# Optimization experiments

Hardware: AMD Instinct MI355X
Metric: run time of the kernel (lower is better)

Reference implementation:

```python
import jax, jax.numpy as jnp
import numpy as np


def _hilbert_d2xy(n, d):
    # standard Hilbert curve: distance d -> (x, y) on n x n grid (n power of 2)
    x = y = 0
    t = d
    s = 1
    while s < n:
        rx = 1 & (t // 2)
        ry = 1 & (t ^ rx)
        if ry == 0:
            if rx == 1:
                x = s - 1 - x
                y = s - 1 - y
            x, y = y, x
        x += s * rx
        y += s * ry
        t //= 4
        s *= 2
    return x, y


def _hilbert_perm(seq_len):
    n = int(round(np.sqrt(seq_len)))
    assert n * n == seq_len
    perm = np.empty(seq_len, dtype=np.int32)
    for d in range(seq_len):
        x, y = _hilbert_d2xy(n, d)
        perm[d] = y * n + x  # linear (row-major) index visited at Hilbert step d
    return perm


def setup_inputs() -> dict:
    key = jax.random.key(0)
    k1, k2, k3 = jax.random.split(key, 3)
    B, S, H, D = 1, 4096, 8, 64
    q = jax.random.normal(k1, (B, S, H, D), dtype=jnp.float32)
    k = jax.random.normal(k2, (B, S, H, D), dtype=jnp.float32)
    v = jax.random.normal(k3, (B, S, H, D), dtype=jnp.float32)
    hilbert_perm = jnp.asarray(_hilbert_perm(S))
    return {"q": q, "k": k, "v": v, "hilbert_perm": hilbert_perm}


def reference(q, k, v, hilbert_perm):
    B, S, H, D = q.shape
    inv_perm = jnp.argsort(hilbert_perm)

    # apply_hilbert_ordering along dim=1 (seq): gather by permutation
    q_o = q[:, hilbert_perm]
    k_o = k[:, hilbert_perm]
    v_o = v[:, hilbert_perm]

    # faithful to original: raw flat reshape of [B,S,H,D] -> [B*H, S, D]
    q_f = q_o.reshape(B * H, S, D)
    k_f = k_o.reshape(B * H, S, D)
    v_f = v_o.reshape(B * H, S, D)

    scale = 1.0 / jnp.sqrt(jnp.asarray(D, dtype=q.dtype))
    scores = jnp.einsum('bsd,btd->bst', q_f, k_f) * scale  # [B*H, S, S]
    attn = jax.nn.softmax(scores, axis=-1)
    out_f = jnp.einsum('bst,btd->bsd', attn, v_f)  # [B*H, S, D]

    out = out_f.reshape(B, H, S, D).transpose(0, 2, 1, 3).reshape(B, S, H, D)
    # inverse Hilbert ordering along dim=1
    return out[:, inv_perm]
```

## Files before the change

### kernel.cpp

```cpp
#include <hip/hip_runtime.h>

typedef _Float16 f16;
typedef _Float16 f16x4 __attribute__((ext_vector_type(4)));
typedef _Float16 f16x8 __attribute__((ext_vector_type(8)));
typedef __fp16 fp16x2 __attribute__((ext_vector_type(2)));
typedef float f32x4 __attribute__((ext_vector_type(4)));

#define MFMA_16x16x32_F16(A, B, C) __builtin_amdgcn_mfma_f32_16x16x32_f16((A), (B), (C), 0, 0, 0)

typedef const __attribute__((address_space(1))) char gchar;
typedef __attribute__((address_space(3))) char lchar;

__device__ __forceinline__ float fexp2(float x) { return __builtin_amdgcn_exp2f(x); }
__device__ __forceinline__ int swzb(int b) { return b ^ ((b >> 3) & 0x70); }

namespace {
constexpr int SB = 4096;
constexpr size_t BB = (size_t)SB * 64 * 2;
}

__global__ __launch_bounds__(256)
void hilbert_prepass_kernel(const float* __restrict__ kp, const float* __restrict__ vp,
                            const int* __restrict__ perm,
                            char* __restrict__ kw, char* __restrict__ vtw)
{
    const int bid = blockIdx.x;
    const int batch = bid & 7;
    const int tile = bid >> 3;
    const int tid = (int)threadIdx.x;
    const int r = tid >> 2;
    const int c4 = tid & 3;

    __shared__ float Vl[64][68];

    const int t = tile * 64 + r;
    const int srow = perm[batch * 512 + (t >> 3)];
    const size_t boff = (size_t)srow * 512 + (t & 7) * 64 + c4 * 16;

    {
        const float* ks = kp + boff;
        const float4 k0 = *(const float4*)(ks + 0);
        const float4 k1 = *(const float4*)(ks + 4);
        const float4 k2 = *(const float4*)(ks + 8);
        const float4 k3 = *(const float4*)(ks + 12);
        f16x8 h0, h1;
        h0[0] = (f16)k0.x; h0[1] = (f16)k0.y; h0[2] = (f16)k0.z; h0[3] = (f16)k0.w;
        h0[4] = (f16)k1.x; h0[5] = (f16)k1.y; h0[6] = (f16)k1.z; h0[7] = (f16)k1.w;
        h1[0] = (f16)k2.x; h1[1] = (f16)k2.y; h1[2] = (f16)k2.z; h1[3] = (f16)k2.w;
        h1[4] = (f16)k3.x; h1[5] = (f16)k3.y; h1[6] = (f16)k3.z; h1[7] = (f16)k3.w;
        char* kt = kw + (size_t)batch * BB + (size_t)tile * 8192;
        const int o = r * 128 + c4 * 32;
        *(f16x8*)(kt + swzb(o)) = h0;
        *(f16x8*)(kt + swzb(o + 16)) = h1;
    }
    {
        const float* vs = vp + boff;
        *(float4*)&Vl[r][c4 * 16 + 0]  = *(const float4*)(vs + 0);
        *(float4*)&Vl[r][c4 * 16 + 4]  = *(const float4*)(vs + 4);
        *(float4*)&Vl[r][c4 * 16 + 8]  = *(const float4*)(vs + 8);
        *(float4*)&Vl[r][c4 * 16 + 12] = *(const float4*)(vs + 12);
    }
    __syncthreads();
    {
        const int d = tid >> 2;
        const int tq = (tid & 3) * 16;
        f16x8 a, b;
#pragma unroll
        for (int j = 0; j < 8; ++j) a[j] = (f16)Vl[tq + j][d];
#pragma unroll
        for (int j = 0; j < 8; ++j) b[j] = (f16)Vl[tq + 8 + j][d];
        char* vt = vtw + (size_t)batch * BB + (size_t)tile * 8192;
        const int o = d * 128 + tq * 2;
        *(f16x8*)(vt + swzb(o)) = a;
        *(f16x8*)(vt + swzb(o + 16)) = b;
    }
}

__global__ __launch_bounds__(512, 4)
void hilbert_attn_kernel(const float* __restrict__ qp,
                         const int* __restrict__ perm,
                         const char* __restrict__ kw, const char* __restrict__ vtw,
                         float* __restrict__ op)
{
    __shared__ __align__(16) char SM[81920];

    const int bid = blockIdx.x;
    const int batch = bid & 7;
    const int qbase = (bid >> 3) * 64;
    const int tid = (int)threadIdx.x;
    const int w = tid >> 6;
    const int lane = tid & 63;
    const int l16 = lane & 15;
    const int g = lane >> 4;
    const int half = w >> 2;
    const int wq = w & 3;
    const int swz = (l16 & 7) << 4;

    f16x8 Qf[2];
    {
        const int t = qbase + wq * 16 + l16;
        const int srow = perm[batch * 512 + (t >> 3)];
        const float* src = qp + (size_t)srow * 512 + (t & 7) * 64 + g * 8;
        constexpr float qscl = 0.125f * 1.44269504088896340736f;
#pragma unroll
        for (int kt = 0; kt < 2; ++kt) {
            const float4 x0 = *(const float4*)(src + 32 * kt);
            const float4 x1 = *(const float4*)(src + 32 * kt + 4);
            f16x8 f;
            f[0] = (f16)(x0.x * qscl); f[1] = (f16)(x0.y * qscl);
            f[2] = (f16)(x0.z * qscl); f[3] = (f16)(x0.w * qscl);
            f[4] = (f16)(x1.x * qscl); f[5] = (f16)(x1.y * qscl);
            f[6] = (f16)(x1.z * qscl); f[7] = (f16)(x1.w * qscl);
            Qf[kt] = f;
        }
    }

    f32x4 oacc[4];
#pragma unroll
    for (int i = 0; i < 4; ++i) oacc[i] = (f32x4){0.f, 0.f, 0.f, 0.f};
    float lrun = 0.f;

    const char* ksrc = kw + (size_t)batch * BB + (size_t)tid * 16;
    const char* vsrc = vtw + (size_t)batch * BB + (size_t)tid * 16;
    char* pbase = &SM[65536 + w * 2048];

    {
        lchar* dst = (lchar*)&SM[w << 10];
        __builtin_amdgcn_global_load_lds((gchar*)(ksrc), dst, 16, 0, 0);
        __builtin_amdgcn_global_load_lds((gchar*)(ksrc + 8192), dst + 8192, 16, 0, 0);
        __builtin_amdgcn_global_load_lds((gchar*)(vsrc), dst + 16384, 16, 0, 0);
        __builtin_amdgcn_global_load_lds((gchar*)(vsrc + 8192), dst + 24576, 16, 0, 0);
    }
    __syncthreads();

    for (int it = 0; it < 32; ++it) {
        const int cur = it & 1;
        const int kbb = cur * 32768 + half * 8192;
        const int vbb = cur * 32768 + 16384 + half * 8192;

        if (it < 31) {
            const size_t go = (size_t)(it + 1) * 16384;
            lchar* dst = (lchar*)&SM[(cur ^ 1) * 32768 + (w << 10)];
            __builtin_amdgcn_global_load_lds((gchar*)(ksrc + go), dst, 16, 0, 0);
            __builtin_amdgcn_global_load_lds((gchar*)(ksrc + go + 8192), dst + 8192, 16, 0, 0);
            __builtin_amdgcn_global_load_lds((gchar*)(vsrc + go), dst + 16384, 16, 0, 0);
            __builtin_amdgcn_global_load_lds((gchar*)(vsrc + go + 8192), dst + 24576, 16, 0, 0);
        }

        f32x4 sa[4];
#pragma unroll
        for (int i = 0; i < 4; ++i) sa[i] = (f32x4){0.f, 0.f, 0.f, 0.f};
#pragma unroll
        for (int kt = 0; kt < 2; ++kt) {
#pragma unroll
            for (int mt = 0; mt < 4; ++mt) {
                const int off = kbb + (l16 + 16 * mt) * 128 + (((g + 4 * kt) * 16) ^ swz);
                const f16x8 kf = *(const f16x8*)&SM[off];
                sa[mt] = MFMA_16x16x32_F16(kf, Qf[kt], sa[mt]);
            }
        }

#pragma unroll
        for (int mt = 0; mt < 4; ++mt) {
            const float p0 = fexp2(sa[mt][0]);
            const float p1 = fexp2(sa[mt][1]);
            const float p2 = fexp2(sa[mt][2]);
            const float p3 = fexp2(sa[mt][3]);
            lrun += (p0 + p1) + (p2 + p3);
            union { f16x4 v; fp16x2 h[2]; } u;
            u.h[0] = __builtin_amdgcn_cvt_pkrtz(p0, p1);
            u.h[1] = __builtin_amdgcn_cvt_pkrtz(p2, p3);
            const int poff = l16 * 128 + (((2 * mt + (g >> 1)) ^ (l16 & 7)) << 4) + (g & 1) * 8;
            *(f16x4*)&pbase[poff] = u.v;
        }

#pragma unroll
        for (int kt = 0; kt < 2; ++kt) {
            const int poff = l16 * 128 + (((g + 4 * kt) ^ (l16 & 7)) << 4);
            const f16x8 pf = *(const f16x8*)&pbase[poff];
#pragma unroll
            for (int mtd = 0; mtd < 4; ++mtd) {
                const int voff = vbb + (l16 + 16 * mtd) * 128 + (((g + 4 * kt) * 16) ^ swz);
                const f16x8 vf = *(const f16x8*)&SM[voff];
                oacc[mtd] = MFMA_16x16x32_F16(vf, pf, oacc[mtd]);
            }
        }

        __syncthreads();
    }

    lrun += __shfl_xor(lrun, 16);
    lrun += __shfl_xor(lrun, 32);

    float* OB = (float*)SM;
    float* ML = (float*)&SM[16384];
    if (w >= 4) {
        float* ob = OB + (w - 4) * 1024;
#pragma unroll
        for (int mtd = 0; mtd < 4; ++mtd)
            *(f32x4*)&ob[l16 * 64 + mtd * 16 + g * 4] = oacc[mtd];
        if (g == 0) ML[(w - 4) * 16 + l16] = lrun;
    }
    __syncthreads();
    if (w < 4) {
        const float linv = 1.f / (lrun + ML[w * 16 + l16]);
        float* ob = OB + w * 1024;

        const int t = qbase + wq * 16 + l16;
        const int srow = perm[t];
        float* dst = op + (size_t)srow * 512 + batch * 64 + 4 * g;
#pragma unroll
        for (int mtd = 0; mtd < 4; ++mtd) {
            const f32x4 o2 = *(const f32x4*)&ob[l16 * 64 + mtd * 16 + g * 4];
            float4 o;
            o.x = (oacc[mtd][0] + o2[0]) * linv;
            o.y = (oacc[mtd][1] + o2[1]) * linv;
            o.z = (oacc[mtd][2] + o2[2]) * linv;
            o.w = (oacc[mtd][3] + o2[3]) * linv;
            *(float4*)(dst + 16 * mtd) = o;
        }
    }
}

extern "C" void kernel_launch(void* const* d_in, const int* in_sizes, int n_in,
                              void* d_out, int out_size, void* d_ws, size_t ws_size,
                              hipStream_t stream) {
    (void)in_sizes; (void)n_in; (void)out_size; (void)ws_size;
    const float* q = (const float*)d_in[0];
    const float* k = (const float*)d_in[1];
    const float* v = (const float*)d_in[2];
    const int* perm = (const int*)d_in[3];
    float* out = (float*)d_out;
    char* kw = (char*)d_ws;
    char* vtw = kw + 8 * BB;
    hipLaunchKernelGGL(hilbert_prepass_kernel, dim3(512), dim3(256), 0, stream,
                       k, v, perm, kw, vtw);
    hipLaunchKernelGGL(hilbert_attn_kernel, dim3(512), dim3(512), 0, stream,
                       q, perm, kw, vtw, out);
}
```

Measured before the change: 60.84 us.

## Process two query sub-tiles per wave to reuse K/V LDS fragments

Each workgroup now handles 128 query rows instead of 64, with every wave computing two 16-row query sub-tiles that share the same K and V fragments read from LDS. The grid halves to 256 blocks, so K/V global-to-LDS traffic per query row and LDS reads per MFMA are halved. The cost is more registers per thread (two sets of accumulators and Q fragments), a larger LDS footprint, a lower occupancy bound, and fewer blocks than a large GPU may have compute units, which can leave some idle.

```diff
diff --git a/kernel.cpp b/kernel.cpp
--- a/kernel.cpp
+++ b/kernel.cpp
@@ -76,17 +76,17 @@
     }
 }
 
-__global__ __launch_bounds__(512, 4)
+__global__ __launch_bounds__(512, 2)
 void hilbert_attn_kernel(const float* __restrict__ qp,
                          const int* __restrict__ perm,
                          const char* __restrict__ kw, const char* __restrict__ vtw,
                          float* __restrict__ op)
 {
-    __shared__ __align__(16) char SM[81920];
+    __shared__ __align__(16) char SM[98304];
 
     const int bid = blockIdx.x;
     const int batch = bid & 7;
-    const int qbase = (bid >> 3) * 64;
+    const int qbase = (bid >> 3) * 128;
     const int tid = (int)threadIdx.x;
     const int w = tid >> 6;
     const int lane = tid & 63;
@@ -96,33 +96,39 @@
     const int wq = w & 3;
     const int swz = (l16 & 7) << 4;
 
-    f16x8 Qf[2];
-    {
-        const int t = qbase + wq * 16 + l16;
-        const int srow = perm[batch * 512 + (t >> 3)];
-        const float* src = qp + (size_t)srow * 512 + (t & 7) * 64 + g * 8;
+    f16x8 Qf0[2], Qf1[2];
+    {
         constexpr float qscl = 0.125f * 1.44269504088896340736f;
 #pragma unroll
-        for (int kt = 0; kt < 2; ++kt) {
-            const float4 x0 = *(const float4*)(src + 32 * kt);
-            const float4 x1 = *(const float4*)(src + 32 * kt + 4);
-            f16x8 f;
-            f[0] = (f16)(x0.x * qscl); f[1] = (f16)(x0.y * qscl);
-            f[2] = (f16)(x0.z * qscl); f[3] = (f16)(x0.w * qscl);
-            f[4] = (f16)(x1.x * qscl); f[5] = (f16)(x1.y * qscl);
-            f[6] = (f16)(x1.z * qscl); f[7] = (f16)(x1.w * qscl);
-            Qf[kt] = f;
-        }
-    }
-
-    f32x4 oacc[4];
-#pragma unroll
-    for (int i = 0; i < 4; ++i) oacc[i] = (f32x4){0.f, 0.f, 0.f, 0.f};
-    float lrun = 0.f;
+        for (int s = 0; s < 2; ++s) {
+            const int t = qbase + wq * 32 + s * 16 + l16;
+            const int srow = perm[batch * 512 + (t >> 3)];
+            const float* src = qp + (size_t)srow * 512 + (t & 7) * 64 + g * 8;
+#pragma unroll
+            for (int kt = 0; kt < 2; ++kt) {
+                const float4 x0 = *(const float4*)(src + 32 * kt);
+                const float4 x1 = *(const float4*)(src + 32 * kt + 4);
+                f16x8 f;
+                f[0] = (f16)(x0.x * qscl); f[1] = (f16)(x0.y * qscl);
+                f[2] = (f16)(x0.z * qscl); f[3] = (f16)(x0.w * qscl);
+                f[4] = (f16)(x1.x * qscl); f[5] = (f16)(x1.y * qscl);
+                f[6] = (f16)(x1.z * qscl); f[7] = (f16)(x1.w * qscl);
+                if (s == 0) Qf0[kt] = f; else Qf1[kt] = f;
+            }
+        }
+    }
+
+    f32x4 oacc0[4], oacc1[4];
+#pragma unroll
+    for (int i = 0; i < 4; ++i) {
+        oacc0[i] = (f32x4){0.f, 0.f, 0.f, 0.f};
+        oacc1[i] = (f32x4){0.f, 0.f, 0.f, 0.f};
+    }
+    float lr0 = 0.f, lr1 = 0.f;
 
     const char* ksrc = kw + (size_t)batch * BB + (size_t)tid * 16;
     const char* vsrc = vtw + (size_t)batch * BB + (size_t)tid * 16;
-    char* pbase = &SM[65536 + w * 2048];
+    char* pbase = &SM[65536 + w * 4096];
 
     {
         lchar* dst = (lchar*)&SM[w << 10];
@@ -147,77 +153,104 @@
             __builtin_amdgcn_global_load_lds((gchar*)(vsrc + go + 8192), dst + 24576, 16, 0, 0);
         }
 
-        f32x4 sa[4];
-#pragma unroll
-        for (int i = 0; i < 4; ++i) sa[i] = (f32x4){0.f, 0.f, 0.f, 0.f};
+        f32x4 sa0[4], sa1[4];
+#pragma unroll
+        for (int i = 0; i < 4; ++i) {
+            sa0[i] = (f32x4){0.f, 0.f, 0.f, 0.f};
+            sa1[i] = (f32x4){0.f, 0.f, 0.f, 0.f};
+        }
 #pragma unroll
         for (int kt = 0; kt < 2; ++kt) {
 #pragma unroll
             for (int mt = 0; mt < 4; ++mt) {
                 const int off = kbb + (l16 + 16 * mt) * 128 + (((g + 4 * kt) * 16) ^ swz);
                 const f16x8 kf = *(const f16x8*)&SM[off];
-                sa[mt] = MFMA_16x16x32_F16(kf, Qf[kt], sa[mt]);
+                sa0[mt] = MFMA_16x16x32_F16(kf, Qf0[kt], sa0[mt]);
+                sa1[mt] = MFMA_16x16x32_F16(kf, Qf1[kt], sa1[mt]);
             }
         }
 
 #pragma unroll
         for (int mt = 0; mt < 4; ++mt) {
-            const float p0 = fexp2(sa[mt][0]);
-            const float p1 = fexp2(sa[mt][1]);
-            const float p2 = fexp2(sa[mt][2]);
-            const float p3 = fexp2(sa[mt][3]);
-            lrun += (p0 + p1) + (p2 + p3);
+            const float a0 = fexp2(sa0[mt][0]);
+            const float a1 = fexp2(sa0[mt][1]);
+            const float a2 = fexp2(sa0[mt][2]);
+            const float a3 = fexp2(sa0[mt][3]);
+            lr0 += (a0 + a1) + (a2 + a3);
             union { f16x4 v; fp16x2 h[2]; } u;
-            u.h[0] = __builtin_amdgcn_cvt_pkrtz(p0, p1);
-            u.h[1] = __builtin_amdgcn_cvt_pkrtz(p2, p3);
+            u.h[0] = __builtin_amdgcn_cvt_pkrtz(a0, a1);
+            u.h[1] = __builtin_amdgcn_cvt_pkrtz(a2, a3);
             const int poff = l16 * 128 + (((2 * mt + (g >> 1)) ^ (l16 & 7)) << 4) + (g & 1) * 8;
             *(f16x4*)&pbase[poff] = u.v;
+
+            const float b0 = fexp2(sa1[mt][0]);
+            const float b1 = fexp2(sa1[mt][1]);
+            const float b2 = fexp2(sa1[mt][2]);
+            const float b3 = fexp2(sa1[mt][3]);
+            lr1 += (b0 + b1) + (b2 + b3);
+            union { f16x4 v; fp16x2 h[2]; } u2;
+            u2.h[0] = __builtin_amdgcn_cvt_pkrtz(b0, b1);
+            u2.h[1] = __builtin_amdgcn_cvt_pkrtz(b2, b3);
+            *(f16x4*)&pbase[2048 + poff] = u2.v;
         }
 
 #pragma unroll
         for (int kt = 0; kt < 2; ++kt) {
             const int poff = l16 * 128 + (((g + 4 * kt) ^ (l16 & 7)) << 4);
-            const f16x8 pf = *(const f16x8*)&pbase[poff];
+            const f16x8 pf0 = *(const f16x8*)&pbase[poff];
+            const f16x8 pf1 = *(const f16x8*)&pbase[2048 + poff];
 #pragma unroll
             for (int mtd = 0; mtd < 4; ++mtd) {
                 const int voff = vbb + (l16 + 16 * mtd) * 128 + (((g + 4 * kt) * 16) ^ swz);
                 const f16x8 vf = *(const f16x8*)&SM[voff];
-                oacc[mtd] = MFMA_16x16x32_F16(vf, pf, oacc[mtd]);
+                oacc0[mtd] = MFMA_16x16x32_F16(vf, pf0, oacc0[mtd]);
+                oacc1[mtd] = MFMA_16x16x32_F16(vf, pf1, oacc1[mtd]);
             }
         }
 
         __syncthreads();
     }
 
-    lrun += __shfl_xor(lrun, 16);
-    lrun += __shfl_xor(lrun, 32);
+    lr0 += __shfl_xor(lr0, 16);
+    lr0 += __shfl_xor(lr0, 32);
+    lr1 += __shfl_xor(lr1, 16);
+    lr1 += __shfl_xor(lr1, 32);
 
     float* OB = (float*)SM;
-    float* ML = (float*)&SM[16384];
+    float* ML = (float*)&SM[32768];
     if (w >= 4) {
-        float* ob = OB + (w - 4) * 1024;
-#pragma unroll
-        for (int mtd = 0; mtd < 4; ++mtd)
-            *(f32x4*)&ob[l16 * 64 + mtd * 16 + g * 4] = oacc[mtd];
-        if (g == 0) ML[(w - 4) * 16 + l16] = lrun;
+        float* ob = OB + wq * 2048;
+#pragma unroll
+        for (int mtd = 0; mtd < 4; ++mtd) {
+            *(f32x4*)&ob[l16 * 64 + mtd * 16 + g * 4] = oacc0[mtd];
+            *(f32x4*)&ob[(16 + l16) * 64 + mtd * 16 + g * 4] = oacc1[mtd];
+        }
+        if (g == 0) {
+            ML[wq * 32 + l16] = lr0;
+            ML[wq * 32 + 16 + l16] = lr1;
+        }
     }
     __syncthreads();
     if (w < 4) {
-        const float linv = 1.f / (lrun + ML[w * 16 + l16]);
-        float* ob = OB + w * 1024;
-
-        const int t = qbase + wq * 16 + l16;
-        const int srow = perm[t];
-        float* dst = op + (size_t)srow * 512 + batch * 64 + 4 * g;
-#pragma unroll
-        for (int mtd = 0; mtd < 4; ++mtd) {
-            const f32x4 o2 = *(const f32x4*)&ob[l16 * 64 + mtd * 16 + g * 4];
-            float4 o;
-            o.x = (oacc[mtd][0] + o2[0]) * linv;
-            o.y = (oacc[mtd][1] + o2[1]) * linv;
-            o.z = (oacc[mtd][2] + o2[2]) * linv;
-            o.w = (oacc[mtd][3] + o2[3]) * linv;
-            *(float4*)(dst + 16 * mtd) = o;
+        float* ob = OB + wq * 2048;
+#pragma unroll
+        for (int s = 0; s < 2; ++s) {
+            const float lmine = (s == 0) ? lr0 : lr1;
+            const float linv = 1.f / (lmine + ML[wq * 32 + s * 16 + l16]);
+            const int t = qbase + wq * 32 + s * 16 + l16;
+            const int srow = perm[t];
+            float* dst = op + (size_t)srow * 512 + batch * 64 + 4 * g;
+#pragma unroll
+            for (int mtd = 0; mtd < 4; ++mtd) {
+                const f32x4 mine = (s == 0) ? oacc0[mtd] : oacc1[mtd];
+                const f32x4 o2 = *(const f32x4*)&ob[(s * 16 + l16) * 64 + mtd * 16 + g * 4];
+                float4 o;
+                o.x = (mine[0] + o2[0]) * linv;
+                o.y = (mine[1] + o2[1]) * linv;
+                o.z = (mine[2] + o2[2]) * linv;
+                o.w = (mine[3] + o2[3]) * linv;
+                *(float4*)(dst + 16 * mtd) = o;
+            }
         }
     }
 }
@@ -235,6 +268,6 @@
     char* vtw = kw + 8 * BB;
     hipLaunchKernelGGL(hilbert_prepass_kernel, dim3(512), dim3(256), 0, stream,
                        k, v, perm, kw, vtw);
-    hipLaunchKernelGGL(hilbert_attn_kernel, dim3(512), dim3(512), 0, stream,
+    hipLaunchKernelGGL(hilbert_attn_kernel, dim3(256), dim3(512), 0, stream,
                        q, perm, kw, vtw, out);
 }
```

Result: faster. 56.74 us (-6.7%).

## Switch attention to 32x32x16 MFMA with register-resident P and split K/V staging

Applied to the files above, without the earlier changes.

Replaces the 16x16x32 MFMA tiling with 32x32x16 MFMAs, doubling the query rows per block to 128 and halving the grid. The V prepass layout is permuted so the exp'd scores can feed the PV MFMA straight from registers, removing the per-wave LDS round trip for P. K and V global-to-LDS staging are now issued separately with explicit vmcnt waits, raw barriers and setprio around the MFMA phases, and the last iteration is peeled. Larger tiles raise register pressure (launch bounds drop to 2 blocks) and leave fewer blocks than CUs.

```diff
diff --git a/kernel.cpp b/kernel.cpp
--- a/kernel.cpp
+++ b/kernel.cpp
@@ -5,8 +5,9 @@
 typedef _Float16 f16x8 __attribute__((ext_vector_type(8)));
 typedef __fp16 fp16x2 __attribute__((ext_vector_type(2)));
 typedef float f32x4 __attribute__((ext_vector_type(4)));
-
-#define MFMA_16x16x32_F16(A, B, C) __builtin_amdgcn_mfma_f32_16x16x32_f16((A), (B), (C), 0, 0, 0)
+typedef float f32x16 __attribute__((ext_vector_type(16)));
+
+#define MFMA32(A, B, C) __builtin_amdgcn_mfma_f32_32x32x16_f16((A), (B), (C), 0, 0, 0)
 
 typedef const __attribute__((address_space(1))) char gchar;
 typedef __attribute__((address_space(3))) char lchar;
@@ -18,6 +19,7 @@
 constexpr int SB = 4096;
 constexpr size_t BB = (size_t)SB * 64 * 2;
 }
+
 
 __global__ __launch_bounds__(256)
 void hilbert_prepass_kernel(const float* __restrict__ kp, const float* __restrict__ vp,
@@ -63,66 +65,126 @@
     __syncthreads();
     {
         const int d = tid >> 2;
-        const int tq = (tid & 3) * 16;
-        f16x8 a, b;
-#pragma unroll
-        for (int j = 0; j < 8; ++j) a[j] = (f16)Vl[tq + j][d];
-#pragma unroll
-        for (int j = 0; j < 8; ++j) b[j] = (f16)Vl[tq + 8 + j][d];
+        const int a = tid & 3;
         char* vt = vtw + (size_t)batch * BB + (size_t)tile * 8192;
-        const int o = d * 128 + tq * 2;
-        *(f16x8*)(vt + swzb(o)) = a;
-        *(f16x8*)(vt + swzb(o + 16)) = b;
+        const int sbase = 32 * (a >> 1) + 16 * (a & 1);
+#pragma unroll
+        for (int gp = 0; gp < 4; ++gp) {
+            f16x4 qv;
+#pragma unroll
+            for (int v = 0; v < 4; ++v) qv[v] = (f16)Vl[16 * a + 4 * gp + v][d];
+            const int slot = sbase + 8 * (gp & 1) + 4 * (gp >> 1);
+            *(f16x4*)(vt + swzb(d * 128 + slot * 2)) = qv;
+        }
     }
 }
 
-__global__ __launch_bounds__(512, 4)
+__global__ __launch_bounds__(512, 2)
 void hilbert_attn_kernel(const float* __restrict__ qp,
                          const int* __restrict__ perm,
                          const char* __restrict__ kw, const char* __restrict__ vtw,
                          float* __restrict__ op)
 {
-    __shared__ __align__(16) char SM[81920];
+    __shared__ __align__(16) char SM[65536];
 
     const int bid = blockIdx.x;
     const int batch = bid & 7;
-    const int qbase = (bid >> 3) * 64;
+    const int qbase = (bid >> 3) * 128;
     const int tid = (int)threadIdx.x;
     const int w = tid >> 6;
     const int lane = tid & 63;
-    const int l16 = lane & 15;
-    const int g = lane >> 4;
+    const int l5 = lane & 31;
+    const int hi = lane >> 5;
+    const int swz = (lane & 7) << 4;
     const int half = w >> 2;
     const int wq = w & 3;
-    const int swz = (l16 & 7) << 4;
-
-    f16x8 Qf[2];
-    {
-        const int t = qbase + wq * 16 + l16;
+
+    const f32x16 Z16 = {0.f, 0.f, 0.f, 0.f, 0.f, 0.f, 0.f, 0.f,
+                        0.f, 0.f, 0.f, 0.f, 0.f, 0.f, 0.f, 0.f};
+
+    f16x8 Qf[4];
+    {
+        constexpr float qscl = 0.125f * 1.44269504088896340736f;
+        const int t = qbase + wq * 32 + l5;
         const int srow = perm[batch * 512 + (t >> 3)];
-        const float* src = qp + (size_t)srow * 512 + (t & 7) * 64 + g * 8;
-        constexpr float qscl = 0.125f * 1.44269504088896340736f;
-#pragma unroll
-        for (int kt = 0; kt < 2; ++kt) {
-            const float4 x0 = *(const float4*)(src + 32 * kt);
-            const float4 x1 = *(const float4*)(src + 32 * kt + 4);
+        const float* src = qp + (size_t)srow * 512 + (t & 7) * 64 + 8 * hi;
+#pragma unroll
+        for (int step = 0; step < 4; ++step) {
+            const float4 x0 = *(const float4*)(src + 16 * step);
+            const float4 x1 = *(const float4*)(src + 16 * step + 4);
             f16x8 f;
             f[0] = (f16)(x0.x * qscl); f[1] = (f16)(x0.y * qscl);
             f[2] = (f16)(x0.z * qscl); f[3] = (f16)(x0.w * qscl);
             f[4] = (f16)(x1.x * qscl); f[5] = (f16)(x1.y * qscl);
             f[6] = (f16)(x1.z * qscl); f[7] = (f16)(x1.w * qscl);
-            Qf[kt] = f;
+            Qf[step] = f;
         }
     }
 
-    f32x4 oacc[4];
-#pragma unroll
-    for (int i = 0; i < 4; ++i) oacc[i] = (f32x4){0.f, 0.f, 0.f, 0.f};
-    float lrun = 0.f;
+    f32x16 oacc[2];
+    oacc[0] = Z16; oacc[1] = Z16;
+    float lr = 0.f;
 
     const char* ksrc = kw + (size_t)batch * BB + (size_t)tid * 16;
     const char* vsrc = vtw + (size_t)batch * BB + (size_t)tid * 16;
-    char* pbase = &SM[65536 + w * 2048];
+
+    union U8 { f16x8 v; fp16x2 h[4]; };
+
+#define STAGE_K(dstbuf, p)                                                           \
+    do {                                                                             \
+        lchar* d_ = (lchar*)&SM[(dstbuf) * 32768 + (w << 10)];                       \
+        const char* s_ = ksrc + (size_t)(p) * 16384;                                 \
+        __builtin_amdgcn_global_load_lds((gchar*)(s_), d_, 16, 0, 0);                \
+        __builtin_amdgcn_global_load_lds((gchar*)(s_ + 8192), d_ + 8192, 16, 0, 0);  \
+    } while (0)
+#define STAGE_V(dstbuf, p)                                                           \
+    do {                                                                             \
+        lchar* d_ = (lchar*)&SM[(dstbuf) * 32768 + 16384 + (w << 10)];               \
+        const char* s_ = vsrc + (size_t)(p) * 16384;                                 \
+        __builtin_amdgcn_global_load_lds((gchar*)(s_), d_, 16, 0, 0);                \
+        __builtin_amdgcn_global_load_lds((gchar*)(s_ + 8192), d_ + 8192, 16, 0, 0);  \
+    } while (0)
+
+#define QK_GRANULE(dst, kbb_, h2)                                                    \
+    do {                                                                             \
+        dst = Z16;                                                                   \
+        _Pragma("unroll")                                                            \
+        for (int step = 0; step < 4; ++step) {                                       \
+            const int off = (kbb_) + (32 * (h2) + l5) * 128 +                        \
+                            ((32 * step + 16 * hi) ^ swz);                           \
+            const f16x8 kf = *(const f16x8*)&SM[off];                                \
+            dst = MFMA32(kf, Qf[step], dst);                                         \
+        }                                                                            \
+    } while (0)
+
+#define SOFTMAX_GRANULE(sa, p0, p1)                                                  \
+    do {                                                                             \
+        float e_[16];                                                                \
+        _Pragma("unroll")                                                            \
+        for (int j = 0; j < 16; ++j) e_[j] = fexp2((sa)[j]);                         \
+        _Pragma("unroll")                                                            \
+        for (int j = 0; j < 16; ++j) lr += e_[j];                                    \
+        _Pragma("unroll")                                                            \
+        for (int i = 0; i < 4; ++i) {                                                \
+            (p0).h[i] = __builtin_amdgcn_cvt_pkrtz(e_[2 * i], e_[2 * i + 1]);        \
+            (p1).h[i] = __builtin_amdgcn_cvt_pkrtz(e_[8 + 2 * i], e_[9 + 2 * i]);    \
+        }                                                                            \
+    } while (0)
+
+#define PV_GRANULE(vbb_, h2, p0, p1)                                                 \
+    do {                                                                             \
+        _Pragma("unroll")                                                            \
+        for (int s = 0; s < 2; ++s) {                                                \
+            const f16x8 pf = s ? (p1).v : (p0).v;                                    \
+            _Pragma("unroll")                                                        \
+            for (int mf = 0; mf < 2; ++mf) {                                         \
+                const int voff = (vbb_) + (32 * mf + l5) * 128 +                     \
+                                 ((64 * (h2) + 32 * s + 16 * hi) ^ swz);             \
+                const f16x8 vf = *(const f16x8*)&SM[voff];                           \
+                oacc[mf] = MFMA32(vf, pf, oacc[mf]);                                 \
+            }                                                                        \
+        }                                                                            \
+    } while (0)
 
     {
         lchar* dst = (lchar*)&SM[w << 10];
@@ -131,94 +193,98 @@
         __builtin_amdgcn_global_load_lds((gchar*)(vsrc), dst + 16384, 16, 0, 0);
         __builtin_amdgcn_global_load_lds((gchar*)(vsrc + 8192), dst + 24576, 16, 0, 0);
     }
-    __syncthreads();
-
-    for (int it = 0; it < 32; ++it) {
+    asm volatile("s_waitcnt vmcnt(0)" ::: "memory");
+    __builtin_amdgcn_s_barrier();
+
+    for (int it = 0; it < 31; ++it) {
         const int cur = it & 1;
         const int kbb = cur * 32768 + half * 8192;
         const int vbb = cur * 32768 + 16384 + half * 8192;
 
-        if (it < 31) {
-            const size_t go = (size_t)(it + 1) * 16384;
-            lchar* dst = (lchar*)&SM[(cur ^ 1) * 32768 + (w << 10)];
-            __builtin_amdgcn_global_load_lds((gchar*)(ksrc + go), dst, 16, 0, 0);
-            __builtin_amdgcn_global_load_lds((gchar*)(ksrc + go + 8192), dst + 8192, 16, 0, 0);
-            __builtin_amdgcn_global_load_lds((gchar*)(vsrc + go), dst + 16384, 16, 0, 0);
-            __builtin_amdgcn_global_load_lds((gchar*)(vsrc + go + 8192), dst + 24576, 16, 0, 0);
-        }
-
-        f32x4 sa[4];
-#pragma unroll
-        for (int i = 0; i < 4; ++i) sa[i] = (f32x4){0.f, 0.f, 0.f, 0.f};
-#pragma unroll
-        for (int kt = 0; kt < 2; ++kt) {
-#pragma unroll
-            for (int mt = 0; mt < 4; ++mt) {
-                const int off = kbb + (l16 + 16 * mt) * 128 + (((g + 4 * kt) * 16) ^ swz);
-                const f16x8 kf = *(const f16x8*)&SM[off];
-                sa[mt] = MFMA_16x16x32_F16(kf, Qf[kt], sa[mt]);
+        STAGE_K(cur ^ 1, it + 1);
+
+        f32x16 sa0, sa1;
+        __builtin_amdgcn_s_setprio(1);
+        QK_GRANULE(sa0, kbb, 0);
+        QK_GRANULE(sa1, kbb, 1);
+        __builtin_amdgcn_s_setprio(0);
+
+        STAGE_V(cur ^ 1, it + 1);
+
+        U8 pa0, pa1, pb0, pb1;
+        SOFTMAX_GRANULE(sa0, pa0, pa1);
+        SOFTMAX_GRANULE(sa1, pb0, pb1);
+
+        asm volatile("s_waitcnt vmcnt(4)" ::: "memory");
+        __builtin_amdgcn_s_barrier();
+
+        __builtin_amdgcn_s_setprio(1);
+        PV_GRANULE(vbb, 0, pa0, pa1);
+        PV_GRANULE(vbb, 1, pb0, pb1);
+        __builtin_amdgcn_s_setprio(0);
+
+        asm volatile("s_waitcnt vmcnt(2)" ::: "memory");
+        __builtin_amdgcn_s_barrier();
+    }
+
+    {
+        const int kbb = 32768 + half * 8192;
+        const int vbb = 32768 + 16384 + half * 8192;
+        f32x16 sa0, sa1;
+        QK_GRANULE(sa0, kbb, 0);
+        QK_GRANULE(sa1, kbb, 1);
+        U8 pa0, pa1, pb0, pb1;
+        SOFTMAX_GRANULE(sa0, pa0, pa1);
+        SOFTMAX_GRANULE(sa1, pb0, pb1);
+        asm volatile("s_waitcnt vmcnt(0)" ::: "memory");
+        __builtin_amdgcn_s_barrier();
+        PV_GRANULE(vbb, 0, pa0, pa1);
+        PV_GRANULE(vbb, 1, pb0, pb1);
+    }
+#undef STAGE_K
+#undef STAGE_V
+#undef QK_GRANULE
+#undef SOFTMAX_GRANULE
+#undef PV_GRANULE
+
+    lr += __shfl_xor(lr, 32);
+
+    __syncthreads();
+
+    float* OB = (float*)SM;
+    float* ML = (float*)&SM[32768];
+    if (w >= 4) {
+        float* ob = OB + wq * 2048;
+#pragma unroll
+        for (int mf = 0; mf < 2; ++mf)
+#pragma unroll
+            for (int q2 = 0; q2 < 4; ++q2) {
+                f32x4 v;
+                v[0] = oacc[mf][4 * q2 + 0]; v[1] = oacc[mf][4 * q2 + 1];
+                v[2] = oacc[mf][4 * q2 + 2]; v[3] = oacc[mf][4 * q2 + 3];
+                *(f32x4*)&ob[l5 * 64 + 32 * mf + 8 * q2 + 4 * hi] = v;
             }
-        }
-
-#pragma unroll
-        for (int mt = 0; mt < 4; ++mt) {
-            const float p0 = fexp2(sa[mt][0]);
-            const float p1 = fexp2(sa[mt][1]);
-            const float p2 = fexp2(sa[mt][2]);
-            const float p3 = fexp2(sa[mt][3]);
-            lrun += (p0 + p1) + (p2 + p3);
-            union { f16x4 v; fp16x2 h[2]; } u;
-            u.h[0] = __builtin_amdgcn_cvt_pkrtz(p0, p1);
-            u.h[1] = __builtin_amdgcn_cvt_pkrtz(p2, p3);
-            const int poff = l16 * 128 + (((2 * mt + (g >> 1)) ^ (l16 & 7)) << 4) + (g & 1) * 8;
-            *(f16x4*)&pbase[poff] = u.v;
-        }
-
-#pragma unroll
-        for (int kt = 0; kt < 2; ++kt) {
-            const int poff = l16 * 128 + (((g + 4 * kt) ^ (l16 & 7)) << 4);
-            const f16x8 pf = *(const f16x8*)&pbase[poff];
-#pragma unroll
-            for (int mtd = 0; mtd < 4; ++mtd) {
-                const int voff = vbb + (l16 + 16 * mtd) * 128 + (((g + 4 * kt) * 16) ^ swz);
-                const f16x8 vf = *(const f16x8*)&SM[voff];
-                oacc[mtd] = MFMA_16x16x32_F16(vf, pf, oacc[mtd]);
-            }
-        }
-
-        __syncthreads();
-    }
-
-    lrun += __shfl_xor(lrun, 16);
-    lrun += __shfl_xor(lrun, 32);
-
-    float* OB = (float*)SM;
-    float* ML = (float*)&SM[16384];
-    if (w >= 4) {
-        float* ob = OB + (w - 4) * 1024;
-#pragma unroll
-        for (int mtd = 0; mtd < 4; ++mtd)
-            *(f32x4*)&ob[l16 * 64 + mtd * 16 + g * 4] = oacc[mtd];
-        if (g == 0) ML[(w - 4) * 16 + l16] = lrun;
+        if (hi == 0) ML[wq * 32 + l5] = lr;
     }
     __syncthreads();
     if (w < 4) {
-        const float linv = 1.f / (lrun + ML[w * 16 + l16]);
-        float* ob = OB + w * 1024;
-
-        const int t = qbase + wq * 16 + l16;
+        float* ob = OB + wq * 2048;
+        const float linv = 1.f / (lr + ML[wq * 32 + l5]);
+        const int t = qbase + wq * 32 + l5;
         const int srow = perm[t];
-        float* dst = op + (size_t)srow * 512 + batch * 64 + 4 * g;
-#pragma unroll
-        for (int mtd = 0; mtd < 4; ++mtd) {
-            const f32x4 o2 = *(const f32x4*)&ob[l16 * 64 + mtd * 16 + g * 4];
-            float4 o;
-            o.x = (oacc[mtd][0] + o2[0]) * linv;
-            o.y = (oacc[mtd][1] + o2[1]) * linv;
-            o.z = (oacc[mtd][2] + o2[2]) * linv;
-            o.w = (oacc[mtd][3] + o2[3]) * linv;
-            *(float4*)(dst + 16 * mtd) = o;
-        }
+        float* dst = op + (size_t)srow * 512 + batch * 64;
+#pragma unroll
+        for (int mf = 0; mf < 2; ++mf)
+#pragma unroll
+            for (int q2 = 0; q2 < 4; ++q2) {
+                const f32x4 o2 = *(const f32x4*)&ob[l5 * 64 + 32 * mf + 8 * q2 + 4 * hi];
+                float4 o;
+                o.x = (oacc[mf][4 * q2 + 0] + o2[0]) * linv;
+                o.y = (oacc[mf][4 * q2 + 1] + o2[1]) * linv;
+                o.z = (oacc[mf][4 * q2 + 2] + o2[2]) * linv;
+                o.w = (oacc[mf][4 * q2 + 3] + o2[3]) * linv;
+                *(float4*)(dst + 32 * mf + 8 * q2 + 4 * hi) = o;
+            }
     }
 }
 
@@ -235,6 +301,6 @@
     char* vtw = kw + 8 * BB;
     hipLaunchKernelGGL(hilbert_prepass_kernel, dim3(512), dim3(256), 0, stream,
                        k, v, perm, kw, vtw);
-    hipLaunchKernelGGL(hilbert_attn_kernel, dim3(512), dim3(512), 0, stream,
+    hipLaunchKernelGGL(hilbert_attn_kernel, dim3(256), dim3(512), 0, stream,
                        q, perm, kw, vtw, out);
 }
```

Measured after the change: 54.23 us. -10.9%, faster.
